# Optimization experiments

Hardware: AMD Instinct MI355X
Metric: run time of the kernel (lower is better)

## Reference

```python
import math
import jax, jax.numpy as jnp
import numpy as np

B, N, D = 8, 2048, 512


def setup_inputs() -> dict:
    key = jax.random.key(0)
    ks = jax.random.split(key, 9)
    s = 1.0 / math.sqrt(D)
    return {
        "x": jax.random.normal(ks[0], (B, N, D), dtype=jnp.float32),
        "adj": jax.random.uniform(ks[1], (B, N, N), dtype=jnp.float32),
        "Wqk": jax.random.normal(ks[2], (D, D), dtype=jnp.float32) * s,
        "bqk": jax.random.normal(ks[3], (D,), dtype=jnp.float32) * s,
        "Wl": jax.random.normal(ks[4], (D, D), dtype=jnp.float32) * s,
        "bl": jax.random.normal(ks[5], (D,), dtype=jnp.float32) * s,
        "Wr": jax.random.normal(ks[6], (D, D), dtype=jnp.float32) * s,
        "Wd": jax.random.normal(ks[7], (D, 1), dtype=jnp.float32),
        "bd": jax.random.normal(ks[8], (D,), dtype=jnp.float32),
    }


def reference(x, adj, Wqk, bqk, Wl, bl, Wr, Wd, bd):
    # degree gating: sigmoid(Linear(rowsum(adj)))
    deg = jnp.sum(adj, axis=-1, keepdims=True)           # [B, N, 1]
    gate = jax.nn.sigmoid(deg * Wd[:, 0] + bd)           # [B, N, D]
    xg = x * gate
    # sigmoid QK features
    QK = jax.nn.sigmoid(xg @ Wqk.T + bqk)                # [B, N, D]
    scores = jnp.einsum("bnd,bmd->bnm", QK, QK) / math.sqrt(D)
    scores = scores * adj                                # adjacency mask
    attn = scores / (jnp.sum(scores, axis=-1, keepdims=True) + 1e-6)
    out = jnp.einsum("bnm,bmd->bnd", attn, xg)           # aggregate values
    out = out @ Wl.T + bl + xg @ Wr.T                    # left + right branch
    return jax.nn.relu(out)
```

## Files before the change

### kernel.cpp

```cpp
#include <hip/hip_runtime.h>
#include <hip/hip_bf16.h>


typedef __bf16 bf16;
typedef __bf16 bf16x2 __attribute__((ext_vector_type(2)));
typedef __bf16 bf16x8 __attribute__((ext_vector_type(8)));
typedef float  f32x4  __attribute__((ext_vector_type(4)));

#define Bb 8
#define Nn 2048
#define Dd 512
#define SMEM_BYTES 33792
#define TILE8_BYTES 49152
#define SMEM8_BYTES (3 * TILE8_BYTES)

__device__ __forceinline__ bf16 to_bf16(float f) { return (bf16)f; }
__device__ __forceinline__ float sigmoidf_(float x) { return 1.0f / (1.0f + __expf(-x)); }

__device__ __forceinline__ void gld16(const void* g, void* l) {
    __builtin_amdgcn_global_load_lds(
        (__attribute__((address_space(1))) void*)(void*)g,
        (__attribute__((address_space(3))) void*)l,
        16, 0, 0);
}

__device__ __forceinline__ void gemm_bt_core(
    const bf16* __restrict__ A, const bf16* __restrict__ Bt,
    int lda, int ldb, int K,
    char* As, char* Bs, f32x4 acc[4][4])
{
    const int tid  = threadIdx.x;
    const int lane = tid & 63;
    const int wave = tid >> 6;
    const int wm = (wave >> 1) << 6;
    const int wn = (wave & 1) << 6;

    for (int kt = 0; kt < K; kt += 64) {
#pragma unroll
        for (int i = 0; i < 4; ++i) {
            int ff   = i * 256 + tid;
            int row  = ff >> 3;
            int slot = ff & 7;
            int gch  = slot ^ (row & 7);
            gld16(A  + (size_t)row * lda + kt + gch * 8, As + ff * 16);
            gld16(Bt + (size_t)row * ldb + kt + gch * 8, Bs + ff * 16);
        }
        __syncthreads();
#pragma unroll
        for (int ks = 0; ks < 2; ++ks) {
            bf16x8 af[4], bfr[4];
#pragma unroll
            for (int mi = 0; mi < 4; ++mi) {
                int row  = wm + mi * 16 + (lane & 15);
                int slot = ((ks << 2) + (lane >> 4)) ^ (row & 7);
                af[mi] = *(const bf16x8*)(As + row * 128 + slot * 16);
            }
#pragma unroll
            for (int ni = 0; ni < 4; ++ni) {
                int row  = wn + ni * 16 + (lane & 15);
                int slot = ((ks << 2) + (lane >> 4)) ^ (row & 7);
                bfr[ni] = *(const bf16x8*)(Bs + row * 128 + slot * 16);
            }
#pragma unroll
            for (int mi = 0; mi < 4; ++mi)
#pragma unroll
                for (int ni = 0; ni < 4; ++ni)
                    acc[mi][ni] = __builtin_amdgcn_mfma_f32_16x16x32_bf16(
                        af[mi], bfr[ni], acc[mi][ni], 0, 0, 0);
        }
        __syncthreads();
    }
}

#define GEMM_PROLOGUE()                                  \
    __shared__ __align__(16) char smem[SMEM_BYTES];      \
    char* As = smem;                                     \
    char* Bs = smem + 16384;                             \
    f32x4 acc[4][4];                                     \
    _Pragma("unroll") for (int mi = 0; mi < 4; ++mi)     \
    _Pragma("unroll") for (int ni = 0; ni < 4; ++ni)     \
        acc[mi][ni] = (f32x4){0.f, 0.f, 0.f, 0.f};

__device__ __forceinline__ void gemm_bt8_core(
    const bf16* __restrict__ A, const bf16* __restrict__ Bt,
    int lda, int ldb, int K, char* smem, f32x4 acc[4][4])
{
    const int tid  = threadIdx.x;
    const int lane = tid & 63;
    const int wave = tid >> 6;
    const int wm = (wave >> 1) << 6;
    const int wn = (wave & 1) << 6;
    const int NT = K >> 6;

    char* bA = smem;
    char* bB = smem + TILE8_BYTES;
    char* bC = smem + 2 * TILE8_BYTES;

    auto stage_half = [&](char* base, int t, int half) {
        const int kt = t << 6;
#pragma unroll
        for (int i = 0; i < 2; ++i) {
            int ff   = (half * 2 + i) * 512 + tid;
            int row  = ff >> 3;
            int slot = ff & 7;
            int gch  = slot ^ (row & 7);
            gld16(A + (size_t)row * lda + kt + gch * 8, base + ff * 16);
        }
        int ff   = half * 512 + tid;
        int row  = ff >> 3;
        int slot = ff & 7;
        int gch  = slot ^ (row & 7);
        gld16(Bt + (size_t)row * ldb + kt + gch * 8, base + 32768 + ff * 16);
    };

    stage_half(bA, 0, 0); stage_half(bA, 0, 1);
    stage_half(bB, 1, 0); stage_half(bB, 1, 1);
    asm volatile("s_waitcnt vmcnt(6)" ::: "memory");
    __builtin_amdgcn_s_barrier();

#pragma unroll 1
    for (int t = 0; t < NT; ++t) {
#pragma unroll
        for (int ks = 0; ks < 2; ++ks) {
            bf16x8 af[4], bfr[4];
#pragma unroll
            for (int mi = 0; mi < 4; ++mi) {
                int row  = wm + mi * 16 + (lane & 15);
                int slot = ((ks << 2) + (lane >> 4)) ^ (row & 7);
                af[mi] = *(const bf16x8*)(bA + row * 128 + slot * 16);
            }
#pragma unroll
            for (int ni = 0; ni < 4; ++ni) {
                int row  = wn + ni * 16 + (lane & 15);
                int slot = ((ks << 2) + (lane >> 4)) ^ (row & 7);
                bfr[ni] = *(const bf16x8*)(bA + 32768 + row * 128 + slot * 16);
            }
            if (t + 2 < NT) stage_half(bC, t + 2, ks);
            __builtin_amdgcn_s_barrier();
            asm volatile("s_waitcnt lgkmcnt(0)" ::: "memory");
            __builtin_amdgcn_sched_barrier(0);
            __builtin_amdgcn_s_setprio(1);
#pragma unroll
            for (int mi = 0; mi < 4; ++mi)
#pragma unroll
                for (int ni = 0; ni < 4; ++ni)
                    acc[mi][ni] = __builtin_amdgcn_mfma_f32_16x16x32_bf16(
                        af[mi], bfr[ni], acc[mi][ni], 0, 0, 0);
            __builtin_amdgcn_s_setprio(0);
            __builtin_amdgcn_sched_barrier(0);
            if (ks == 1) {
                if (t + 2 < NT)      asm volatile("s_waitcnt vmcnt(6)" ::: "memory");
                else if (t + 1 < NT) asm volatile("s_waitcnt vmcnt(0)" ::: "memory");
            }
            __builtin_amdgcn_s_barrier();
        }
        char* tmp = bA; bA = bB; bB = bC; bC = tmp;
    }
}

template <typename F>
__device__ __forceinline__ void epilogue_rt8(f32x4 acc[4][4], char* smem, F&& emit)
{
    const int tid  = threadIdx.x;
    const int lane = tid & 63;
    const int wave = tid >> 6;
    const int wm4 = wave >> 1;
    const int wn  = (wave & 1) << 6;
    const int cq = lane >> 4;
    const int cl = lane & 15;
    float* t = (float*)smem;
    const int chunk = tid & 15;
    const int rbase = tid >> 4;
#pragma unroll
    for (int ph = 0; ph < 4; ++ph) {
        __syncthreads();
        if (wm4 == ph) {
#pragma unroll
            for (int mi = 0; mi < 4; ++mi)
#pragma unroll
                for (int ni = 0; ni < 4; ++ni)
#pragma unroll
                    for (int r = 0; r < 4; ++r) {
                        int lr = mi * 16 + cq * 4 + r;
                        int lc = wn + ni * 16 + cl;
                        t[lr * 132 + lc] = acc[mi][ni][r];
                    }
        }
        __syncthreads();
#pragma unroll
        for (int rr = 0; rr < 2; ++rr) {
            int lr = rr * 32 + rbase;
            f32x4 a = *(const f32x4*)&t[lr * 132 + chunk * 8];
            f32x4 b = *(const f32x4*)&t[lr * 132 + chunk * 8 + 4];
            float v[8] = {a[0], a[1], a[2], a[3], b[0], b[1], b[2], b[3]};
            emit(ph * 64 + lr, chunk * 8, v);
        }
    }
}

__global__ __launch_bounds__(256) void k_castw(
    const float* __restrict__ Wqk, const float* __restrict__ Wl,
    const float* __restrict__ Wr,
    bf16* __restrict__ Wqkb, bf16* __restrict__ Wlb, bf16* __restrict__ Wrb)
{
    int i = blockIdx.x * 256 + threadIdx.x;
    Wqkb[i] = to_bf16(Wqk[i]);
    Wlb[i]  = to_bf16(Wl[i]);
    Wrb[i]  = to_bf16(Wr[i]);
}

__global__ __launch_bounds__(256) void k_gate(
    const float* __restrict__ x, const float* __restrict__ adj,
    const float* __restrict__ Wd, const float* __restrict__ bd,
    bf16* __restrict__ xg)
{
    const int rowg = blockIdx.x;
    const float4* arow = (const float4*)(adj + (size_t)rowg * Nn);
    float4 v0 = arow[threadIdx.x];
    float4 v1 = arow[threadIdx.x + 256];
    float s = v0.x + v0.y + v0.z + v0.w + v1.x + v1.y + v1.z + v1.w;
#pragma unroll
    for (int off = 32; off > 0; off >>= 1) s += __shfl_down(s, off, 64);
    __shared__ float red[4];
    if ((threadIdx.x & 63) == 0) red[threadIdx.x >> 6] = s;
    __syncthreads();
    const float deg = red[0] + red[1] + red[2] + red[3];
    const int d2 = threadIdx.x;
    float2 xv  = ((const float2*)(x + (size_t)rowg * Dd))[d2];
    float2 wd  = ((const float2*)Wd)[d2];
    float2 bd2 = ((const float2*)bd)[d2];
    bf16x2 o;
    o[0] = to_bf16(xv.x * sigmoidf_(deg * wd.x + bd2.x));
    o[1] = to_bf16(xv.y * sigmoidf_(deg * wd.y + bd2.y));
    *(bf16x2*)(xg + (size_t)rowg * Dd + d2 * 2) = o;
}

__global__ __launch_bounds__(256) void k_transpose(
    const bf16* __restrict__ xg, bf16* __restrict__ xgT)
{
    const int b = blockIdx.z, nt = blockIdx.y, dt = blockIdx.x;
    __shared__ bf16 tile[64][66];
    const int c = threadIdx.x & 63, r0 = threadIdx.x >> 6;
    const bf16* src = xg + ((size_t)b * Nn + nt * 64) * Dd + dt * 64;
#pragma unroll
    for (int i = 0; i < 16; ++i) {
        int r = i * 4 + r0;
        tile[r][c] = src[(size_t)r * Dd + c];
    }
    __syncthreads();
    bf16* dst = xgT + ((size_t)b * Dd + dt * 64) * Nn + nt * 64;
#pragma unroll
    for (int i = 0; i < 16; ++i) {
        int r = i * 4 + r0;
        dst[(size_t)r * Nn + c] = tile[c][r];
    }
}

__global__ __launch_bounds__(512) void k_qk_gemm8(
    const bf16* __restrict__ xg, const bf16* __restrict__ Wqkb,
    const float* __restrict__ bqk, bf16* __restrict__ QK)
{
    extern __shared__ __align__(16) char smem[];
    const int blockRow = blockIdx.y * 256;
    const int blockCol = blockIdx.x * 128;
    f32x4 acc[4][4];
#pragma unroll
    for (int mi = 0; mi < 4; ++mi)
#pragma unroll
        for (int ni = 0; ni < 4; ++ni) acc[mi][ni] = (f32x4){0.f, 0.f, 0.f, 0.f};
    gemm_bt8_core(xg + (size_t)blockRow * Dd, Wqkb + (size_t)blockCol * Dd,
                  Dd, Dd, Dd, smem, acc);
    epilogue_rt8(acc, smem, [&](int lr, int lc, float* v) {
        int c = blockCol + lc;
        float4 b0 = *(const float4*)(bqk + c);
        float4 b1 = *(const float4*)(bqk + c + 4);
        float bb[8] = {b0.x, b0.y, b0.z, b0.w, b1.x, b1.y, b1.z, b1.w};
        bf16x8 o;
#pragma unroll
        for (int j = 0; j < 8; ++j) o[j] = to_bf16(sigmoidf_(v[j] + bb[j]));
        *(bf16x8*)(QK + (size_t)(blockRow + lr) * Dd + c) = o;
    });
}

__global__ __launch_bounds__(256) void k_s_gemm(
    const bf16* __restrict__ QK, const float* __restrict__ adj,
    bf16* __restrict__ S, float* __restrict__ denom)
{
    const int b = blockIdx.y;
    int t = blockIdx.x, i = 0;
    while (t >= 16 - i) { t -= 16 - i; ++i; }
    const int j = i + t;
    const int rowI = i * 128, rowJ = j * 128;
    const bf16* Qb = QK + (size_t)b * Nn * Dd;
    GEMM_PROLOGUE();
    gemm_bt_core(Qb + (size_t)rowI * Dd, Qb + (size_t)rowJ * Dd,
                 Dd, Dd, Dd, As, Bs, acc);
    const float scale = 0.044194173824159216f;

    const int tid  = threadIdx.x;
    const int lane = tid & 63;
    const int wave = tid >> 6;
    const int wm = (wave >> 1) << 6;
    const int wn = (wave & 1) << 6;
    const int cq = lane >> 4;
    const int cl = lane & 15;
    float* tls = (float*)smem;
    const int chunk = tid & 15;
    const int rbase = tid >> 4;

    auto store_side = [&](int blockRow, int blockCol, bool trans) {
#pragma unroll
        for (int ph = 0; ph < 2; ++ph) {
            __syncthreads();
            if (!trans) {
                if ((wave >> 1) == ph) {
#pragma unroll
                    for (int mi = 0; mi < 4; ++mi)
#pragma unroll
                        for (int ni = 0; ni < 4; ++ni)
#pragma unroll
                            for (int r = 0; r < 4; ++r)
                                tls[(mi * 16 + cq * 4 + r) * 132 + wn + ni * 16 + cl]
                                    = acc[mi][ni][r];
                }
            } else {
                if ((wave & 1) == ph) {
#pragma unroll
                    for (int mi = 0; mi < 4; ++mi)
#pragma unroll
                        for (int ni = 0; ni < 4; ++ni)
#pragma unroll
                            for (int r = 0; r < 4; ++r)
                                tls[(ni * 16 + cl) * 132 + wm + mi * 16 + cq * 4 + r]
                                    = acc[mi][ni][r];
                }
            }
            __syncthreads();
#pragma unroll
            for (int rr = 0; rr < 4; ++rr) {
                int lr = rr * 16 + rbase;
                f32x4 a = *(const f32x4*)&tls[lr * 132 + chunk * 8];
                f32x4 c4 = *(const f32x4*)&tls[lr * 132 + chunk * 8 + 4];
                float v[8] = {a[0], a[1], a[2], a[3], c4[0], c4[1], c4[2], c4[3]};
                int gRow = blockRow + ph * 64 + lr;
                size_t base = ((size_t)b * Nn + gRow) * Nn + blockCol + chunk * 8;
                float4 a0 = *(const float4*)(adj + base);
                float4 a1 = *(const float4*)(adj + base + 4);
                float aa[8] = {a0.x, a0.y, a0.z, a0.w, a1.x, a1.y, a1.z, a1.w};
                bf16x8 o;
                float ds = 0.f;
#pragma unroll
                for (int jj = 0; jj < 8; ++jj) {
                    float s = v[jj] * scale * aa[jj];
                    bf16 sb = to_bf16(s);
                    o[jj] = sb;
                    ds += (float)sb;
                }
                *(bf16x8*)(S + base) = o;
#pragma unroll
                for (int off = 8; off > 0; off >>= 1) ds += __shfl_xor(ds, off, 16);
                if ((tid & 15) == 0) atomicAdd(&denom[b * Nn + gRow], ds);
            }
        }
    };
    store_side(rowI, rowJ, false);
    if (i != j) store_side(rowJ, rowI, true);
}

__global__ __launch_bounds__(512) void k_h_gemm8(
    const bf16* __restrict__ S, const bf16* __restrict__ xgT,
    const float* __restrict__ denom, bf16* __restrict__ h)
{
    extern __shared__ __align__(16) char smem[];
    const int id  = blockIdx.x;
    const int b   = id & 7;
    const int pos = id >> 3;
    const int blockRow = (pos >> 2) * 256;
    const int blockCol = (pos & 3) * 128;
    f32x4 acc[4][4];
#pragma unroll
    for (int mi = 0; mi < 4; ++mi)
#pragma unroll
        for (int ni = 0; ni < 4; ++ni) acc[mi][ni] = (f32x4){0.f, 0.f, 0.f, 0.f};
    gemm_bt8_core(S + ((size_t)b * Nn + blockRow) * Nn,
                  xgT + ((size_t)b * Dd + blockCol) * Nn,
                  Nn, Nn, Nn, smem, acc);
    epilogue_rt8(acc, smem, [&](int lr, int lc, float* v) {
        int gRow = blockRow + lr;
        float inv = 1.0f / (denom[b * Nn + gRow] + 1e-6f);
        bf16x8 o;
#pragma unroll
        for (int j = 0; j < 8; ++j) o[j] = to_bf16(v[j] * inv);
        *(bf16x8*)(h + ((size_t)b * Nn + gRow) * Dd + blockCol + lc) = o;
    });
}

__global__ __launch_bounds__(512) void k_out_gemm8(
    const bf16* __restrict__ h, const bf16* __restrict__ xg,
    const bf16* __restrict__ Wlb, const bf16* __restrict__ Wrb,
    const float* __restrict__ bl, float* __restrict__ out)
{
    extern __shared__ __align__(16) char smem[];
    const int blockRow = blockIdx.y * 256;
    const int blockCol = blockIdx.x * 128;
    f32x4 acc[4][4];
#pragma unroll
    for (int mi = 0; mi < 4; ++mi)
#pragma unroll
        for (int ni = 0; ni < 4; ++ni) acc[mi][ni] = (f32x4){0.f, 0.f, 0.f, 0.f};
    gemm_bt8_core(h  + (size_t)blockRow * Dd, Wlb + (size_t)blockCol * Dd,
                  Dd, Dd, Dd, smem, acc);
    gemm_bt8_core(xg + (size_t)blockRow * Dd, Wrb + (size_t)blockCol * Dd,
                  Dd, Dd, Dd, smem, acc);
    epilogue_rt8(acc, smem, [&](int lr, int lc, float* v) {
        int c = blockCol + lc;
        float4 b0 = *(const float4*)(bl + c);
        float4 b1 = *(const float4*)(bl + c + 4);
        float bb[8] = {b0.x, b0.y, b0.z, b0.w, b1.x, b1.y, b1.z, b1.w};
        float4 o0, o1;
        o0.x = fmaxf(v[0] + bb[0], 0.f); o0.y = fmaxf(v[1] + bb[1], 0.f);
        o0.z = fmaxf(v[2] + bb[2], 0.f); o0.w = fmaxf(v[3] + bb[3], 0.f);
        o1.x = fmaxf(v[4] + bb[4], 0.f); o1.y = fmaxf(v[5] + bb[5], 0.f);
        o1.z = fmaxf(v[6] + bb[6], 0.f); o1.w = fmaxf(v[7] + bb[7], 0.f);
        float* p = out + (size_t)(blockRow + lr) * Dd + c;
        *(float4*)p = o0;
        *(float4*)(p + 4) = o1;
    });
}

extern "C" void kernel_launch(void* const* d_in, const int* in_sizes, int n_in,
                              void* d_out, int out_size, void* d_ws, size_t ws_size,
                              hipStream_t stream) {
    const float* x   = (const float*)d_in[0];
    const float* adj = (const float*)d_in[1];
    const float* Wqk = (const float*)d_in[2];
    const float* bqk = (const float*)d_in[3];
    const float* Wl  = (const float*)d_in[4];
    const float* bl  = (const float*)d_in[5];
    const float* Wr  = (const float*)d_in[6];
    const float* Wd  = (const float*)d_in[7];
    const float* bd  = (const float*)d_in[8];
    float* out = (float*)d_out;

    char* ws = (char*)d_ws;
    bf16* xg   = (bf16*)ws;  ws += (size_t)Bb * Nn * Dd * 2;
    bf16* xgT  = (bf16*)ws;  ws += (size_t)Bb * Dd * Nn * 2;
    bf16* QK   = (bf16*)ws;  ws += (size_t)Bb * Nn * Dd * 2;
    bf16* S    = (bf16*)ws;  ws += (size_t)Bb * Nn * Nn * 2;
    bf16* Wqkb = (bf16*)ws;  ws += (size_t)Dd * Dd * 2;
    bf16* Wlb  = (bf16*)ws;  ws += (size_t)Dd * Dd * 2;
    bf16* Wrb  = (bf16*)ws;  ws += (size_t)Dd * Dd * 2;
    float* denom = (float*)ws; ws += (size_t)Bb * Nn * 4;
    bf16* h = QK;

    static bool attr_done = false;
    if (!attr_done) {
        hipFuncSetAttribute((const void*)k_qk_gemm8,
                            hipFuncAttributeMaxDynamicSharedMemorySize, SMEM8_BYTES);
        hipFuncSetAttribute((const void*)k_h_gemm8,
                            hipFuncAttributeMaxDynamicSharedMemorySize, SMEM8_BYTES);
        hipFuncSetAttribute((const void*)k_out_gemm8,
                            hipFuncAttributeMaxDynamicSharedMemorySize, SMEM8_BYTES);
        attr_done = true;
    }

    hipMemsetAsync(denom, 0, (size_t)Bb * Nn * sizeof(float), stream);
    k_castw<<<dim3(1024), 256, 0, stream>>>(Wqk, Wl, Wr, Wqkb, Wlb, Wrb);
    k_gate<<<dim3(Bb * Nn), 256, 0, stream>>>(x, adj, Wd, bd, xg);
    k_transpose<<<dim3(Dd / 64, Nn / 64, Bb), 256, 0, stream>>>(xg, xgT);
    k_qk_gemm8<<<dim3(Dd / 128, (Bb * Nn) / 256), 512, SMEM8_BYTES, stream>>>(xg, Wqkb, bqk, QK);
    k_s_gemm<<<dim3(136, Bb), 256, 0, stream>>>(QK, adj, S, denom);
    k_h_gemm8<<<dim3(256), 512, SMEM8_BYTES, stream>>>(S, xgT, denom, h);
    k_out_gemm8<<<dim3(Dd / 128, (Bb * Nn) / 256), 512, SMEM8_BYTES, stream>>>(h, xg, Wlb, Wrb, bl, out);
}
```

Measured before the change: 380.0 us.

## Restructure GEMM pipeline into full-tile stages, merge dual GEMMs, fuse prep kernels

The GEMM core now stages a whole K-tile per iteration instead of two half-stages. It splits the LDS fragment reads so the second half loads while the first half's MFMAs run, and it can chain two A/B operand pairs through one continuous pipeline. This lets the output GEMM run its left and right branches without draining and restarting the prefetch. The weight cast and denominator memset are folded into the gate kernel, removing two launches. The trade-offs are more registers for the double fragment sets and a per-tile operand-select branch.

```diff
diff --git a/kernel.cpp b/kernel.cpp
--- a/kernel.cpp
+++ b/kernel.cpp
@@ -82,78 +82,106 @@
         acc[mi][ni] = (f32x4){0.f, 0.f, 0.f, 0.f};
 
 __device__ __forceinline__ void gemm_bt8_core(
-    const bf16* __restrict__ A, const bf16* __restrict__ Bt,
-    int lda, int ldb, int K, char* smem, f32x4 acc[4][4])
+    const bf16* __restrict__ A0, const bf16* __restrict__ B0,
+    int lda0, int ldb0, int nt0,
+    const bf16* __restrict__ A1, const bf16* __restrict__ B1,
+    int lda1, int ldb1, int nt1,
+    char* smem, f32x4 acc[4][4])
 {
     const int tid  = threadIdx.x;
     const int lane = tid & 63;
     const int wave = tid >> 6;
     const int wm = (wave >> 1) << 6;
     const int wn = (wave & 1) << 6;
-    const int NT = K >> 6;
+    const int NT = nt0 + nt1;
 
     char* bA = smem;
     char* bB = smem + TILE8_BYTES;
     char* bC = smem + 2 * TILE8_BYTES;
 
-    auto stage_half = [&](char* base, int t, int half) {
-        const int kt = t << 6;
-#pragma unroll
-        for (int i = 0; i < 2; ++i) {
-            int ff   = (half * 2 + i) * 512 + tid;
+    auto stage_tile = [&](char* base, int t) {
+        const bf16* A  = (t < nt0) ? A0 : A1;
+        const bf16* Bt = (t < nt0) ? B0 : B1;
+        const int lda  = (t < nt0) ? lda0 : lda1;
+        const int ldb  = (t < nt0) ? ldb0 : ldb1;
+        const int kt   = ((t < nt0) ? t : t - nt0) << 6;
+#pragma unroll
+        for (int i = 0; i < 4; ++i) {
+            int ff   = i * 512 + tid;
             int row  = ff >> 3;
             int slot = ff & 7;
             int gch  = slot ^ (row & 7);
             gld16(A + (size_t)row * lda + kt + gch * 8, base + ff * 16);
         }
-        int ff   = half * 512 + tid;
-        int row  = ff >> 3;
-        int slot = ff & 7;
-        int gch  = slot ^ (row & 7);
-        gld16(Bt + (size_t)row * ldb + kt + gch * 8, base + 32768 + ff * 16);
+#pragma unroll
+        for (int i = 0; i < 2; ++i) {
+            int ff   = i * 512 + tid;
+            int row  = ff >> 3;
+            int slot = ff & 7;
+            int gch  = slot ^ (row & 7);
+            gld16(Bt + (size_t)row * ldb + kt + gch * 8, base + 32768 + ff * 16);
+        }
     };
 
-    stage_half(bA, 0, 0); stage_half(bA, 0, 1);
-    stage_half(bB, 1, 0); stage_half(bB, 1, 1);
+    stage_tile(bA, 0);
+    stage_tile(bB, 1);
     asm volatile("s_waitcnt vmcnt(6)" ::: "memory");
     __builtin_amdgcn_s_barrier();
 
 #pragma unroll 1
     for (int t = 0; t < NT; ++t) {
-#pragma unroll
-        for (int ks = 0; ks < 2; ++ks) {
-            bf16x8 af[4], bfr[4];
-#pragma unroll
-            for (int mi = 0; mi < 4; ++mi) {
-                int row  = wm + mi * 16 + (lane & 15);
-                int slot = ((ks << 2) + (lane >> 4)) ^ (row & 7);
-                af[mi] = *(const bf16x8*)(bA + row * 128 + slot * 16);
-            }
-#pragma unroll
-            for (int ni = 0; ni < 4; ++ni) {
-                int row  = wn + ni * 16 + (lane & 15);
-                int slot = ((ks << 2) + (lane >> 4)) ^ (row & 7);
-                bfr[ni] = *(const bf16x8*)(bA + 32768 + row * 128 + slot * 16);
-            }
-            if (t + 2 < NT) stage_half(bC, t + 2, ks);
-            __builtin_amdgcn_s_barrier();
-            asm volatile("s_waitcnt lgkmcnt(0)" ::: "memory");
-            __builtin_amdgcn_sched_barrier(0);
-            __builtin_amdgcn_s_setprio(1);
-#pragma unroll
-            for (int mi = 0; mi < 4; ++mi)
-#pragma unroll
-                for (int ni = 0; ni < 4; ++ni)
-                    acc[mi][ni] = __builtin_amdgcn_mfma_f32_16x16x32_bf16(
-                        af[mi], bfr[ni], acc[mi][ni], 0, 0, 0);
-            __builtin_amdgcn_s_setprio(0);
-            __builtin_amdgcn_sched_barrier(0);
-            if (ks == 1) {
-                if (t + 2 < NT)      asm volatile("s_waitcnt vmcnt(6)" ::: "memory");
-                else if (t + 1 < NT) asm volatile("s_waitcnt vmcnt(0)" ::: "memory");
-            }
-            __builtin_amdgcn_s_barrier();
-        }
+        bf16x8 af0[4], bf0[4], af1[4], bf1[4];
+#pragma unroll
+        for (int mi = 0; mi < 4; ++mi) {
+            int row  = wm + mi * 16 + (lane & 15);
+            int slot = (lane >> 4) ^ (row & 7);
+            af0[mi] = *(const bf16x8*)(bA + row * 128 + slot * 16);
+        }
+#pragma unroll
+        for (int ni = 0; ni < 4; ++ni) {
+            int row  = wn + ni * 16 + (lane & 15);
+            int slot = (lane >> 4) ^ (row & 7);
+            bf0[ni] = *(const bf16x8*)(bA + 32768 + row * 128 + slot * 16);
+        }
+        if (t + 2 < NT) stage_tile(bC, t + 2);
+        __builtin_amdgcn_s_barrier();
+        asm volatile("s_waitcnt lgkmcnt(0)" ::: "memory");
+        __builtin_amdgcn_sched_barrier(0);
+#pragma unroll
+        for (int mi = 0; mi < 4; ++mi) {
+            int row  = wm + mi * 16 + (lane & 15);
+            int slot = (4 + (lane >> 4)) ^ (row & 7);
+            af1[mi] = *(const bf16x8*)(bA + row * 128 + slot * 16);
+        }
+#pragma unroll
+        for (int ni = 0; ni < 4; ++ni) {
+            int row  = wn + ni * 16 + (lane & 15);
+            int slot = (4 + (lane >> 4)) ^ (row & 7);
+            bf1[ni] = *(const bf16x8*)(bA + 32768 + row * 128 + slot * 16);
+        }
+        __builtin_amdgcn_sched_barrier(0);
+        __builtin_amdgcn_s_setprio(1);
+#pragma unroll
+        for (int mi = 0; mi < 4; ++mi)
+#pragma unroll
+            for (int ni = 0; ni < 4; ++ni)
+                acc[mi][ni] = __builtin_amdgcn_mfma_f32_16x16x32_bf16(
+                    af0[mi], bf0[ni], acc[mi][ni], 0, 0, 0);
+        __builtin_amdgcn_s_setprio(0);
+        asm volatile("s_waitcnt lgkmcnt(0)" ::: "memory");
+        __builtin_amdgcn_sched_barrier(0);
+        __builtin_amdgcn_s_setprio(1);
+#pragma unroll
+        for (int mi = 0; mi < 4; ++mi)
+#pragma unroll
+            for (int ni = 0; ni < 4; ++ni)
+                acc[mi][ni] = __builtin_amdgcn_mfma_f32_16x16x32_bf16(
+                    af1[mi], bf1[ni], acc[mi][ni], 0, 0, 0);
+        __builtin_amdgcn_s_setprio(0);
+        __builtin_amdgcn_sched_barrier(0);
+        if (t + 2 < NT)      asm volatile("s_waitcnt vmcnt(6)" ::: "memory");
+        else if (t + 1 < NT) asm volatile("s_waitcnt vmcnt(0)" ::: "memory");
+        __builtin_amdgcn_s_barrier();
         char* tmp = bA; bA = bB; bB = bC; bC = tmp;
     }
 }
@@ -198,34 +226,35 @@
     }
 }
 
-__global__ __launch_bounds__(256) void k_castw(
-    const float* __restrict__ Wqk, const float* __restrict__ Wl,
-    const float* __restrict__ Wr,
-    bf16* __restrict__ Wqkb, bf16* __restrict__ Wlb, bf16* __restrict__ Wrb)
-{
-    int i = blockIdx.x * 256 + threadIdx.x;
-    Wqkb[i] = to_bf16(Wqk[i]);
-    Wlb[i]  = to_bf16(Wl[i]);
-    Wrb[i]  = to_bf16(Wr[i]);
-}
-
 __global__ __launch_bounds__(256) void k_gate(
     const float* __restrict__ x, const float* __restrict__ adj,
     const float* __restrict__ Wd, const float* __restrict__ bd,
-    bf16* __restrict__ xg)
+    const float* __restrict__ Wqk, const float* __restrict__ Wl,
+    const float* __restrict__ Wr,
+    bf16* __restrict__ xg, bf16* __restrict__ Wqkb, bf16* __restrict__ Wlb,
+    bf16* __restrict__ Wrb, float* __restrict__ denom)
 {
     const int rowg = blockIdx.x;
+    const int tid  = threadIdx.x;
+    if (tid < 48) {
+        int idx = rowg * 48 + tid;
+        if (idx < 262144)      Wqkb[idx]          = to_bf16(Wqk[idx]);
+        else if (idx < 524288) Wlb[idx - 262144]  = to_bf16(Wl[idx - 262144]);
+        else                   Wrb[idx - 524288]  = to_bf16(Wr[idx - 524288]);
+    }
+    if (tid == 63) denom[rowg] = 0.f;
+
     const float4* arow = (const float4*)(adj + (size_t)rowg * Nn);
-    float4 v0 = arow[threadIdx.x];
-    float4 v1 = arow[threadIdx.x + 256];
+    float4 v0 = arow[tid];
+    float4 v1 = arow[tid + 256];
     float s = v0.x + v0.y + v0.z + v0.w + v1.x + v1.y + v1.z + v1.w;
 #pragma unroll
     for (int off = 32; off > 0; off >>= 1) s += __shfl_down(s, off, 64);
     __shared__ float red[4];
-    if ((threadIdx.x & 63) == 0) red[threadIdx.x >> 6] = s;
+    if ((tid & 63) == 0) red[tid >> 6] = s;
     __syncthreads();
     const float deg = red[0] + red[1] + red[2] + red[3];
-    const int d2 = threadIdx.x;
+    const int d2 = tid;
     float2 xv  = ((const float2*)(x + (size_t)rowg * Dd))[d2];
     float2 wd  = ((const float2*)Wd)[d2];
     float2 bd2 = ((const float2*)bd)[d2];
@@ -269,7 +298,8 @@
 #pragma unroll
         for (int ni = 0; ni < 4; ++ni) acc[mi][ni] = (f32x4){0.f, 0.f, 0.f, 0.f};
     gemm_bt8_core(xg + (size_t)blockRow * Dd, Wqkb + (size_t)blockCol * Dd,
-                  Dd, Dd, Dd, smem, acc);
+                  Dd, Dd, 8,
+                  xg, Wqkb, Dd, Dd, 0, smem, acc);
     epilogue_rt8(acc, smem, [&](int lr, int lc, float* v) {
         int c = blockCol + lc;
         float4 b0 = *(const float4*)(bqk + c);
@@ -384,7 +414,8 @@
         for (int ni = 0; ni < 4; ++ni) acc[mi][ni] = (f32x4){0.f, 0.f, 0.f, 0.f};
     gemm_bt8_core(S + ((size_t)b * Nn + blockRow) * Nn,
                   xgT + ((size_t)b * Dd + blockCol) * Nn,
-                  Nn, Nn, Nn, smem, acc);
+                  Nn, Nn, 32,
+                  S, xgT, Nn, Nn, 0, smem, acc);
     epilogue_rt8(acc, smem, [&](int lr, int lc, float* v) {
         int gRow = blockRow + lr;
         float inv = 1.0f / (denom[b * Nn + gRow] + 1e-6f);
@@ -409,9 +440,9 @@
 #pragma unroll
         for (int ni = 0; ni < 4; ++ni) acc[mi][ni] = (f32x4){0.f, 0.f, 0.f, 0.f};
     gemm_bt8_core(h  + (size_t)blockRow * Dd, Wlb + (size_t)blockCol * Dd,
-                  Dd, Dd, Dd, smem, acc);
-    gemm_bt8_core(xg + (size_t)blockRow * Dd, Wrb + (size_t)blockCol * Dd,
-                  Dd, Dd, Dd, smem, acc);
+                  Dd, Dd, 8,
+                  xg + (size_t)blockRow * Dd, Wrb + (size_t)blockCol * Dd,
+                  Dd, Dd, 8, smem, acc);
     epilogue_rt8(acc, smem, [&](int lr, int lc, float* v) {
         int c = blockCol + lc;
         float4 b0 = *(const float4*)(bl + c);
@@ -464,9 +495,8 @@
         attr_done = true;
     }
 
-    hipMemsetAsync(denom, 0, (size_t)Bb * Nn * sizeof(float), stream);
-    k_castw<<<dim3(1024), 256, 0, stream>>>(Wqk, Wl, Wr, Wqkb, Wlb, Wrb);
-    k_gate<<<dim3(Bb * Nn), 256, 0, stream>>>(x, adj, Wd, bd, xg);
+    k_gate<<<dim3(Bb * Nn), 256, 0, stream>>>(x, adj, Wd, bd, Wqk, Wl, Wr,
+                                              xg, Wqkb, Wlb, Wrb, denom);
     k_transpose<<<dim3(Dd / 64, Nn / 64, Bb), 256, 0, stream>>>(xg, xgT);
     k_qk_gemm8<<<dim3(Dd / 128, (Bb * Nn) / 256), 512, SMEM8_BYTES, stream>>>(xg, Wqkb, bqk, QK);
     k_s_gemm<<<dim3(136, Bb), 256, 0, stream>>>(QK, adj, S, denom);
```

Result: no change. 381.0 us (+0.3%).
